# Performance work log

Measured on AMD Instinct MI355X. Metric: run time of the kernel, lower is better.

Reference implementation:

```python
import jax, jax.numpy as jnp
import numpy as np


def setup_inputs() -> dict:
    key = jax.random.key(0)
    k1, k2, k3, k4 = jax.random.split(key, 4)
    B, C, H, W = 4, 64, 128, 256
    Cout, kH, kW = 64, 3, 3
    x = jax.random.normal(k1, (B, C, H, W), dtype=jnp.float32)
    # offset layout: channel 2*(i*kW+j) = dy, 2*(i*kW+j)+1 = dx (deformable_groups=1)
    offset = jax.random.normal(k2, (B, 2 * kH * kW, H, W), dtype=jnp.float32)
    weight = jax.random.normal(k3, (Cout, C, kH, kW), dtype=jnp.float32) * 0.05
    bias = jax.random.normal(k4, (Cout,), dtype=jnp.float32) * 0.05
    return {"x": x, "offset": offset, "weight": weight, "bias": bias}


STRIDE, PAD, DIL = 1, 1, 1


def _deform_conv(x, offset, weight, bias):
    B, C, H, W = x.shape
    Cout, Cin, kH, kW = weight.shape
    K = kH * kW
    Ho = (H + 2 * PAD - DIL * (kH - 1) - 1) // STRIDE + 1
    Wo = (W + 2 * PAD - DIL * (kW - 1) - 1) // STRIDE + 1

    hs = (jnp.arange(Ho) * STRIDE - PAD).astype(jnp.float32)  # [Ho]
    ws = (jnp.arange(Wo) * STRIDE - PAD).astype(jnp.float32)  # [Wo]
    ki, kj = jnp.meshgrid(jnp.arange(kH), jnp.arange(kW), indexing="ij")
    ki = (ki.reshape(K) * DIL).astype(jnp.float32)  # [K]
    kj = (kj.reshape(K) * DIL).astype(jnp.float32)

    off = offset.reshape(B, K, 2, Ho, Wo)
    dy, dx = off[:, :, 0], off[:, :, 1]  # [B,K,Ho,Wo]
    py = hs[None, None, :, None] + ki[None, :, None, None] + dy  # [B,K,Ho,Wo]
    px = ws[None, None, None, :] + kj[None, :, None, None] + dx

    y0 = jnp.floor(py)
    x0 = jnp.floor(px)
    ly = py - y0
    lx = px - x0
    y0i = y0.astype(jnp.int32)
    x0i = x0.astype(jnp.int32)

    def gather(xb, yi, xi):
        # xb: [C,H,W]; yi, xi: [K,Ho,Wo]; zero for out-of-bounds corners
        valid = (yi >= 0) & (yi < H) & (xi >= 0) & (xi < W)
        yc = jnp.clip(yi, 0, H - 1)
        xc = jnp.clip(xi, 0, W - 1)
        idx = (yc * W + xc).reshape(-1)
        g = jnp.take(xb.reshape(C, H * W), idx, axis=1).reshape(C, K, Ho, Wo)
        return g * valid[None].astype(xb.dtype)

    gather_b = jax.vmap(gather)
    corners = [
        (y0i, x0i, (1.0 - ly) * (1.0 - lx)),
        (y0i, x0i + 1, (1.0 - ly) * lx),
        (y0i + 1, x0i, ly * (1.0 - lx)),
        (y0i + 1, x0i + 1, ly * lx),
    ]
    vals = jnp.zeros((B, C, K, Ho, Wo), dtype=x.dtype)
    for yi, xi, w in corners:
        vals = vals + gather_b(x, yi, xi) * w[:, None]  # broadcast over C

    out = jnp.einsum("bckhw,ock->bohw", vals, weight.reshape(Cout, Cin, K))
    return out + bias[None, :, None, None]


def reference(x, offset, weight, bias):
    return _deform_conv(x, offset, weight, bias)
```

## Files before the change

### kernel.cpp

```cpp
#include <hip/hip_runtime.h>

typedef float floatx4 __attribute__((ext_vector_type(4)));
typedef _Float16 half2v __attribute__((ext_vector_type(2)));
typedef _Float16 half8 __attribute__((ext_vector_type(8)));

#define Hh 128
#define Ww 256
#define Cc 64
#define COUT 64
#define Bb 4
#define HW (Hh*Ww)
#define VP 74

__global__ void wtrans(const float* __restrict__ src, unsigned short* __restrict__ dst) {
    int i = blockIdx.x * 256 + threadIdx.x;
    if (i >= COUT * Cc * 9) return;
    int kt = i % 9, c = (i / 9) % Cc, o = i / (9 * Cc);
    _Float16 hv = (_Float16)src[i];
    dst[(kt * COUT + o) * Cc + c] = *(unsigned short*)&hv;
}

__global__ void xtrans(const float* __restrict__ src, _Float16* __restrict__ dst) {
    __shared__ unsigned short T[128][VP];
    const int wh = blockIdx.x, h = blockIdx.y, b = blockIdx.z;
    const int tid = threadIdx.x;
    const int wl = tid & 127;
    const int ch = tid >> 7;
    const float* sp = src + ((b * Cc + ch * 32) * Hh + h) * Ww + wh * 128 + wl;
#pragma unroll
    for (int c2 = 0; c2 < 16; ++c2) {
        const float v0 = sp[(2 * c2) * HW];
        const float v1 = sp[(2 * c2 + 1) * HW];
        half2v hv; hv.x = (_Float16)v0; hv.y = (_Float16)v1;
        *(unsigned*)&T[wl][ch * 32 + 2 * c2] = *(unsigned*)&hv;
    }
    __syncthreads();
    uint4* drow = (uint4*)(dst + ((size_t)(b * Hh + h) * Ww + wh * 128) * 64);
#pragma unroll
    for (int j = 0; j < 4; ++j) {
        const int idx = j * 256 + tid;
        drow[idx] = *(const uint4*)&T[idx >> 3][(idx & 7) * 8];
    }
}

__device__ __forceinline__ void lds_barrier() {
    asm volatile("s_waitcnt lgkmcnt(0)\n\ts_barrier" ::: "memory");
}

struct Tap {
    half2v W00, W01, W10, W11;
    int a00, a01, a10, a11;
};

__device__ __forceinline__ void tap_setup(int kt, int h, int w, float dy, float dx,
                                          int cg, Tap& t) {
    const int ki = kt / 3, kj = kt % 3;
    const float py = (float)(h - 1 + ki) + dy;
    const float px = (float)(w - 1 + kj) + dx;
    const float y0f = floorf(py), x0f = floorf(px);
    const int y0 = (int)y0f, x0 = (int)x0f;
    const float ly = py - y0f, lx = px - x0f;
    const int y1 = y0 + 1, x1 = x0 + 1;
    const bool vy0 = ((unsigned)y0 < Hh), vy1 = ((unsigned)y1 < Hh);
    const bool vx0 = ((unsigned)x0 < Ww), vx1 = ((unsigned)x1 < Ww);
    const float w00 = (vy0 && vx0) ? (1.f - ly) * (1.f - lx) : 0.f;
    const float w01 = (vy0 && vx1) ? (1.f - ly) * lx : 0.f;
    const float w10 = (vy1 && vx0) ? ly * (1.f - lx) : 0.f;
    const float w11 = (vy1 && vx1) ? ly * lx : 0.f;
    _Float16 h00 = (_Float16)w00, h01 = (_Float16)w01;
    _Float16 h10 = (_Float16)w10, h11 = (_Float16)w11;
    t.W00.x = h00; t.W00.y = h00;  t.W01.x = h01; t.W01.y = h01;
    t.W10.x = h10; t.W10.y = h10;  t.W11.x = h11; t.W11.y = h11;
    const int y0c = min(max(y0, 0), Hh - 1), y1c = min(max(y1, 0), Hh - 1);
    const int x0c = min(max(x0, 0), Ww - 1), x1c = min(max(x1, 0), Ww - 1);
    t.a00 = (y0c * Ww + x0c) * 8 + cg;
    t.a01 = (y0c * Ww + x1c) * 8 + cg;
    t.a10 = (y1c * Ww + x0c) * 8 + cg;
    t.a11 = (y1c * Ww + x1c) * 8 + cg;
}

__device__ __forceinline__ void tap_load(const uint4* __restrict__ xb4, const Tap& t,
                                         unsigned (&pf)[16]) {
    *(uint4*)&pf[0]  = xb4[t.a00];
    *(uint4*)&pf[4]  = xb4[t.a01];
    *(uint4*)&pf[8]  = xb4[t.a10];
    *(uint4*)&pf[12] = xb4[t.a11];
}

__device__ __forceinline__ void tap_store(const Tap& t, const unsigned (&pf)[16],
                                          unsigned short* __restrict__ vrow) {
    unsigned o[4];
#pragma unroll
    for (int s = 0; s < 4; ++s) {
        half2v v = (*(const half2v*)&pf[s])      * t.W00
                 + (*(const half2v*)&pf[4 + s])  * t.W01
                 + (*(const half2v*)&pf[8 + s])  * t.W10
                 + (*(const half2v*)&pf[12 + s]) * t.W11;
        o[s] = *(unsigned*)&v;
    }
    uint4 u; u.x = o[0]; u.y = o[1]; u.z = o[2]; u.w = o[3];
    *(uint4*)vrow = u;
}

__device__ __forceinline__ void mfma_tap(const unsigned short* __restrict__ wk,
                                         const unsigned short* __restrict__ Vbuf,
                                         int wv, int ln, floatx4 (&acc)[2]) {
    const int nt = wv & 1;
    const int mb = (wv >> 1) * 2;
#pragma unroll
    for (int g = 0; g < 2; ++g) {
        const int pp = nt * 16 + (ln & 15);
        half8 bfrag = *(const half8*)&Vbuf[pp * VP + g * 32 + (ln >> 4) * 8];
#pragma unroll
        for (int mi = 0; mi < 2; ++mi) {
            const int oo = (mb + mi) * 16 + (ln & 15);
            half8 afrag = *(const half8*)(wk + oo * Cc + g * 32 + (ln >> 4) * 8);
            acc[mi] = __builtin_amdgcn_mfma_f32_16x16x32_f16(afrag, bfrag, acc[mi], 0, 0, 0);
        }
    }
}

template<int KT>
__device__ __forceinline__ void pipe_iter(
    const uint4* __restrict__ xb4, const float* __restrict__ offb,
    const unsigned short* __restrict__ wb,
    const unsigned short* __restrict__ Vb0, const unsigned short* __restrict__ Vb1,
    unsigned short* __restrict__ vrow0, unsigned short* __restrict__ vrow1,
    int h, int w, int cg, int wv, int ln,
    Tap& tp0, Tap& tp1, unsigned (&pf0)[16], unsigned (&pf1)[16],
    float& dy0, float& dx0, float& dy1, float& dx1,
    floatx4 (&acc)[2])
{
    constexpr int S = KT & 1, T = 1 - S;
    Tap& tpS = S ? tp1 : tp0;
    Tap& tpT = S ? tp0 : tp1;
    unsigned (&pfS)[16] = S ? pf1 : pf0;
    unsigned (&pfT)[16] = S ? pf0 : pf1;

    if constexpr (KT < 8) {
        const float dyn = T ? dy1 : dy0;
        const float dxn = T ? dx1 : dx0;
        tap_setup(KT + 1, h, w, dyn, dxn, cg, tpT);
    }
    mfma_tap(wb + (KT - 1) * COUT * Cc, T ? Vb1 : Vb0, wv, ln, acc);
    if constexpr (KT < 8) tap_load(xb4, tpT, pfT);
    tap_store(tpS, pfS, S ? vrow1 : vrow0);
    if constexpr (KT + 3 <= 8) {
        (T ? dy1 : dy0) = offb[(2 * (KT + 3)) * HW];
        (T ? dx1 : dx0) = offb[(2 * (KT + 3) + 1) * HW];
    }
    lds_barrier();
}

__launch_bounds__(256, 6)
__global__ void dcn_mfma(const _Float16* __restrict__ xn,
                         const float* __restrict__ offset,
                         const unsigned short* __restrict__ wb,
                         const float* __restrict__ bias,
                         float* __restrict__ out) {
    __shared__ unsigned short V[2][32 * VP];

    const int tid = threadIdx.x;
    const int p   = tid >> 3;
    const int cg  = tid & 7;
    const int wv  = tid >> 6;
    const int ln  = tid & 63;

    const int b  = blockIdx.z;
    const int h  = blockIdx.y;
    const int w0 = blockIdx.x * 32;
    const int w  = w0 + p;

    const uint4* xb4  = (const uint4*)(xn + (size_t)b * HW * 64);
    const float* offb = offset + b * 18 * HW + h * Ww + w;
    unsigned short* vrow0 = &V[0][p * VP + cg * 8];
    unsigned short* vrow1 = &V[1][p * VP + cg * 8];

    floatx4 acc[2];
    acc[0] = (floatx4)0.f; acc[1] = (floatx4)0.f;

    unsigned pf0[16], pf1[16];
    Tap tp0, tp1;

    float dy0 = offb[0],        dx0 = offb[HW];
    float dy1 = offb[2 * HW],   dx1 = offb[3 * HW];
    tap_setup(0, h, w, dy0, dx0, cg, tp0);
    tap_load(xb4, tp0, pf0);
    tap_setup(1, h, w, dy1, dx1, cg, tp1);
    tap_load(xb4, tp1, pf1);
    dy0 = offb[4 * HW]; dx0 = offb[5 * HW];
    dy1 = offb[6 * HW]; dx1 = offb[7 * HW];
    tap_store(tp0, pf0, vrow0);
    lds_barrier();

#define PI(K) pipe_iter<K>(xb4, offb, wb, V[0], V[1], vrow0, vrow1, h, w, cg, wv, ln, \
                           tp0, tp1, pf0, pf1, dy0, dx0, dy1, dx1, acc)
    PI(1); PI(2); PI(3); PI(4); PI(5); PI(6); PI(7); PI(8);
#undef PI

    mfma_tap(wb + 8 * COUT * Cc, V[0], wv, ln, acc);

    float* outp = out + b * COUT * HW + h * Ww;
    const int nt = wv & 1;
    const int mb = (wv >> 1) * 2;
    const int col = w0 + nt * 16 + (ln & 15);
#pragma unroll
    for (int mi = 0; mi < 2; ++mi)
#pragma unroll
        for (int r = 0; r < 4; ++r) {
            const int o = (mb + mi) * 16 + (ln >> 4) * 4 + r;
            outp[o * HW + col] = acc[mi][r] + bias[o];
        }
}

extern "C" void kernel_launch(void* const* d_in, const int* in_sizes, int n_in,
                              void* d_out, int out_size, void* d_ws, size_t ws_size,
                              hipStream_t stream) {
    const float* x      = (const float*)d_in[0];
    const float* offset = (const float*)d_in[1];
    const float* weight = (const float*)d_in[2];
    const float* bias   = (const float*)d_in[3];
    float* out = (float*)d_out;

    _Float16* xn = (_Float16*)d_ws;
    unsigned short* wb = (unsigned short*)((char*)d_ws + (size_t)Bb * HW * Cc * 2);

    wtrans<<<dim3((COUT * Cc * 9 + 255) / 256), 256, 0, stream>>>(weight, wb);
    xtrans<<<dim3(2, Hh, Bb), 256, 0, stream>>>(x, xn);
    dcn_mfma<<<dim3(Ww / 32, Hh, Bb), 256, 0, stream>>>(xn, offset, wb, bias, out);
}
```

Before: 179.2 us.

## Prefetch weight fragments into registers one tap ahead and fuse prep kernels

```diff
diff --git a/kernel.cpp b/kernel.cpp
--- a/kernel.cpp
+++ b/kernel.cpp
@@ -12,21 +12,23 @@
 #define HW (Hh*Ww)
 #define VP 74
 
-__global__ void wtrans(const float* __restrict__ src, unsigned short* __restrict__ dst) {
-    int i = blockIdx.x * 256 + threadIdx.x;
-    if (i >= COUT * Cc * 9) return;
-    int kt = i % 9, c = (i / 9) % Cc, o = i / (9 * Cc);
-    _Float16 hv = (_Float16)src[i];
-    dst[(kt * COUT + o) * Cc + c] = *(unsigned short*)&hv;
-}
-
-__global__ void xtrans(const float* __restrict__ src, _Float16* __restrict__ dst) {
+__global__ void prep(const float* __restrict__ x, const float* __restrict__ wsrc,
+                     _Float16* __restrict__ xn, unsigned short* __restrict__ wdst) {
+    const int bx = blockIdx.x, h = blockIdx.y, b = blockIdx.z;
+    const int tid = threadIdx.x;
+    if (bx == 2) {
+        const int i = (h + Hh * b) * 72 + tid;
+        if (tid < 72) {
+            const int kt = i % 9, c = (i / 9) % Cc, o = i / (9 * Cc);
+            _Float16 hv = (_Float16)wsrc[i];
+            wdst[(kt * COUT + o) * Cc + c] = *(unsigned short*)&hv;
+        }
+        return;
+    }
     __shared__ unsigned short T[128][VP];
-    const int wh = blockIdx.x, h = blockIdx.y, b = blockIdx.z;
-    const int tid = threadIdx.x;
     const int wl = tid & 127;
     const int ch = tid >> 7;
-    const float* sp = src + ((b * Cc + ch * 32) * Hh + h) * Ww + wh * 128 + wl;
+    const float* sp = x + ((b * Cc + ch * 32) * Hh + h) * Ww + bx * 128 + wl;
 #pragma unroll
     for (int c2 = 0; c2 < 16; ++c2) {
         const float v0 = sp[(2 * c2) * HW];
@@ -35,7 +37,7 @@
         *(unsigned*)&T[wl][ch * 32 + 2 * c2] = *(unsigned*)&hv;
     }
     __syncthreads();
-    uint4* drow = (uint4*)(dst + ((size_t)(b * Hh + h) * Ww + wh * 128) * 64);
+    uint4* drow = (uint4*)(xn + ((size_t)(b * Hh + h) * Ww + bx * 128) * 64);
 #pragma unroll
     for (int j = 0; j < 4; ++j) {
         const int idx = j * 256 + tid;
@@ -87,6 +89,14 @@
     *(uint4*)&pf[12] = xb4[t.a11];
 }
 
+__device__ __forceinline__ void wf_load(const unsigned short* __restrict__ wt,
+                                        half8 (&WF)[4]) {
+    WF[0] = *(const half8*)(wt);
+    WF[1] = *(const half8*)(wt + 16 * Cc);
+    WF[2] = *(const half8*)(wt + 32);
+    WF[3] = *(const half8*)(wt + 16 * Cc + 32);
+}
+
 __device__ __forceinline__ void tap_store(const Tap& t, const unsigned (&pf)[16],
                                           unsigned short* __restrict__ vrow) {
     unsigned o[4];
@@ -102,57 +112,46 @@
     *(uint4*)vrow = u;
 }
 
-__device__ __forceinline__ void mfma_tap(const unsigned short* __restrict__ wk,
+__device__ __forceinline__ void mfma_tap(const half8 (&WF)[4],
                                          const unsigned short* __restrict__ Vbuf,
-                                         int wv, int ln, floatx4 (&acc)[2]) {
-    const int nt = wv & 1;
-    const int mb = (wv >> 1) * 2;
+                                         int nt, int ln, floatx4 (&acc)[2]) {
 #pragma unroll
     for (int g = 0; g < 2; ++g) {
         const int pp = nt * 16 + (ln & 15);
         half8 bfrag = *(const half8*)&Vbuf[pp * VP + g * 32 + (ln >> 4) * 8];
-#pragma unroll
-        for (int mi = 0; mi < 2; ++mi) {
-            const int oo = (mb + mi) * 16 + (ln & 15);
-            half8 afrag = *(const half8*)(wk + oo * Cc + g * 32 + (ln >> 4) * 8);
-            acc[mi] = __builtin_amdgcn_mfma_f32_16x16x32_f16(afrag, bfrag, acc[mi], 0, 0, 0);
-        }
+        acc[0] = __builtin_amdgcn_mfma_f32_16x16x32_f16(WF[2 * g],     bfrag, acc[0], 0, 0, 0);
+        acc[1] = __builtin_amdgcn_mfma_f32_16x16x32_f16(WF[2 * g + 1], bfrag, acc[1], 0, 0, 0);
     }
 }
 
 template<int KT>
 __device__ __forceinline__ void pipe_iter(
     const uint4* __restrict__ xb4, const float* __restrict__ offb,
-    const unsigned short* __restrict__ wb,
-    const unsigned short* __restrict__ Vb0, const unsigned short* __restrict__ Vb1,
+    const unsigned short* __restrict__ wfb,
+    const unsigned short* __restrict__ V0, const unsigned short* __restrict__ V1,
     unsigned short* __restrict__ vrow0, unsigned short* __restrict__ vrow1,
-    int h, int w, int cg, int wv, int ln,
+    int h, int w, int cg, int nt, int ln,
     Tap& tp0, Tap& tp1, unsigned (&pf0)[16], unsigned (&pf1)[16],
+    half8 (&WF0)[4], half8 (&WF1)[4],
     float& dy0, float& dx0, float& dy1, float& dx1,
     floatx4 (&acc)[2])
 {
     constexpr int S = KT & 1, T = 1 - S;
-    Tap& tpS = S ? tp1 : tp0;
-    Tap& tpT = S ? tp0 : tp1;
-    unsigned (&pfS)[16] = S ? pf1 : pf0;
-    unsigned (&pfT)[16] = S ? pf0 : pf1;
-
+    wf_load(wfb + KT * COUT * Cc, S ? WF1 : WF0);
     if constexpr (KT < 8) {
-        const float dyn = T ? dy1 : dy0;
-        const float dxn = T ? dx1 : dx0;
-        tap_setup(KT + 1, h, w, dyn, dxn, cg, tpT);
-    }
-    mfma_tap(wb + (KT - 1) * COUT * Cc, T ? Vb1 : Vb0, wv, ln, acc);
-    if constexpr (KT < 8) tap_load(xb4, tpT, pfT);
-    tap_store(tpS, pfS, S ? vrow1 : vrow0);
+        tap_setup(KT + 1, h, w, T ? dy1 : dy0, T ? dx1 : dx0, cg, T ? tp1 : tp0);
+        tap_load(xb4, T ? tp1 : tp0, T ? pf1 : pf0);
+    }
     if constexpr (KT + 3 <= 8) {
         (T ? dy1 : dy0) = offb[(2 * (KT + 3)) * HW];
         (T ? dx1 : dx0) = offb[(2 * (KT + 3) + 1) * HW];
     }
+    mfma_tap(T ? WF1 : WF0, T ? V1 : V0, nt, ln, acc);
+    tap_store(S ? tp1 : tp0, S ? pf1 : pf0, S ? vrow1 : vrow0);
     lds_barrier();
 }
 
-__launch_bounds__(256, 6)
+__launch_bounds__(256, 4)
 __global__ void dcn_mfma(const _Float16* __restrict__ xn,
                          const float* __restrict__ offset,
                          const unsigned short* __restrict__ wb,
@@ -176,14 +175,20 @@
     unsigned short* vrow0 = &V[0][p * VP + cg * 8];
     unsigned short* vrow1 = &V[1][p * VP + cg * 8];
 
+    const int nt = wv & 1;
+    const int mb = (wv >> 1) * 2;
+    const unsigned short* wfb = wb + (mb * 16 + (ln & 15)) * Cc + (ln >> 4) * 8;
+
     floatx4 acc[2];
     acc[0] = (floatx4)0.f; acc[1] = (floatx4)0.f;
 
     unsigned pf0[16], pf1[16];
+    half8 WF0[4], WF1[4];
     Tap tp0, tp1;
 
     float dy0 = offb[0],        dx0 = offb[HW];
     float dy1 = offb[2 * HW],   dx1 = offb[3 * HW];
+    wf_load(wfb, WF0);
     tap_setup(0, h, w, dy0, dx0, cg, tp0);
     tap_load(xb4, tp0, pf0);
     tap_setup(1, h, w, dy1, dx1, cg, tp1);
@@ -193,16 +198,14 @@
     tap_store(tp0, pf0, vrow0);
     lds_barrier();
 
-#define PI(K) pipe_iter<K>(xb4, offb, wb, V[0], V[1], vrow0, vrow1, h, w, cg, wv, ln, \
-                           tp0, tp1, pf0, pf1, dy0, dx0, dy1, dx1, acc)
+#define PI(K) pipe_iter<K>(xb4, offb, wfb, V[0], V[1], vrow0, vrow1, h, w, cg, nt, ln, \
+                           tp0, tp1, pf0, pf1, WF0, WF1, dy0, dx0, dy1, dx1, acc)
     PI(1); PI(2); PI(3); PI(4); PI(5); PI(6); PI(7); PI(8);
 #undef PI
 
-    mfma_tap(wb + 8 * COUT * Cc, V[0], wv, ln, acc);
+    mfma_tap(WF0, V[0], nt, ln, acc);
 
     float* outp = out + b * COUT * HW + h * Ww;
-    const int nt = wv & 1;
-    const int mb = (wv >> 1) * 2;
     const int col = w0 + nt * 16 + (ln & 15);
 #pragma unroll
     for (int mi = 0; mi < 2; ++mi)
@@ -225,7 +228,6 @@
     _Float16* xn = (_Float16*)d_ws;
     unsigned short* wb = (unsigned short*)((char*)d_ws + (size_t)Bb * HW * Cc * 2);
 
-    wtrans<<<dim3((COUT * Cc * 9 + 255) / 256), 256, 0, stream>>>(weight, wb);
-    xtrans<<<dim3(2, Hh, Bb), 256, 0, stream>>>(x, xn);
+    prep<<<dim3(3, Hh, Bb), 256, 0, stream>>>(x, weight, xn, wb);
     dcn_mfma<<<dim3(Ww / 32, Hh, Bb), 256, 0, stream>>>(xn, offset, wb, bias, out);
 }
```

Result: no change. 176.3 us (-1.6%).
